# Kernel tuning notes

Measured on AMD Instinct MI355X. Metric: run time of the kernel, lower is better.

## Reference

```python
import jax, jax.numpy as jnp
import numpy as np

N_NODES = 100000
N_EDGES = 800000
D_IN = 256
D_HID = 256
D_OUT = 64
HEADS = 1
ALPHA = 0.5          # TransConv residual weight
GRAPH_WEIGHT = 0.8   # _SGFormer aggregate='add' weight
LN_EPS = 1e-5
BN_EPS = 1e-5


def layer_norm(x, g, b):
    mu = x.mean(-1, keepdims=True)
    var = ((x - mu) ** 2).mean(-1, keepdims=True)
    return (x - mu) * jax.lax.rsqrt(var + LN_EPS) * g + b


def full_attention_conv(qs, ks, vs):
    # qs, ks, vs: [N, H, C]; normalization is by the GLOBAL Frobenius norm
    qs = qs / jnp.linalg.norm(qs)
    ks = ks / jnp.linalg.norm(ks)
    N = qs.shape[0]
    kvs = jnp.einsum('lhm,lhd->hmd', ks, vs)                     # [H,C,C]
    attention_num = jnp.einsum('nhm,hmd->nhd', qs, kvs) + N * vs  # [N,H,C]
    ks_sum = ks.sum(axis=0)                                      # [H,C]
    normalizer = jnp.einsum('nhm,hm->nh', qs, ks_sum)[..., None] + N
    return attention_num / normalizer


def gcn_conv(x, src, dst, w, b, n):
    # PyG GCNConv: h = x @ W; add self-loops; D^-1/2 (A+I) D^-1/2 h; + bias
    h = x @ w
    loop = jnp.arange(n)
    s = jnp.concatenate([src, loop])
    d = jnp.concatenate([dst, loop])
    deg = jax.ops.segment_sum(jnp.ones_like(s, dtype=h.dtype), d, num_segments=n)
    dinv = jnp.where(deg > 0, jax.lax.rsqrt(jnp.maximum(deg, 1e-12)), 0.0)
    norm = dinv[s] * dinv[d]
    out = jax.ops.segment_sum(h[s] * norm[:, None], d, num_segments=n)
    return out + b


def setup_inputs() -> dict:
    key = jax.random.key(0)
    ks = jax.random.split(key, 24)
    f32 = jnp.float32
    def lin(k, fi, fo):
        s = 1.0 / np.sqrt(fi)
        kw, kb = jax.random.split(k)
        return (jax.random.uniform(kw, (fi, fo), f32, -s, s),
                jax.random.uniform(kb, (fo,), f32, -s, s))
    x = jax.random.normal(ks[0], (N_NODES, D_IN), f32)
    edge_index = jax.random.randint(ks[1], (2, N_EDGES), 0, N_NODES, jnp.int64)
    fc0_w, fc0_b = lin(ks[2], D_IN, D_HID)
    wq0_w, wq0_b = lin(ks[3], D_HID, D_HID * HEADS)
    wk0_w, wk0_b = lin(ks[4], D_HID, D_HID * HEADS)
    wv0_w, wv0_b = lin(ks[5], D_HID, D_HID * HEADS)
    wq1_w, wq1_b = lin(ks[6], D_HID, D_HID * HEADS)
    wk1_w, wk1_b = lin(ks[7], D_HID, D_HID * HEADS)
    wv1_w, wv1_b = lin(ks[8], D_HID, D_HID * HEADS)
    gcn_w0, gcn_b0 = lin(ks[9], D_IN, D_HID)
    gcn_w1, gcn_b1 = lin(ks[10], D_HID, D_HID)
    fc_w, fc_b = lin(ks[11], D_HID, D_OUT)
    ones = jnp.ones((D_HID,), f32)
    zeros = jnp.zeros((D_HID,), f32)
    return dict(
        x=x, edge_index=edge_index,
        fc0_w=fc0_w, fc0_b=fc0_b, ln0_g=ones, ln0_b=zeros,
        wq0_w=wq0_w, wq0_b=wq0_b, wk0_w=wk0_w, wk0_b=wk0_b, wv0_w=wv0_w, wv0_b=wv0_b,
        ln1_g=ones, ln1_b=zeros,
        wq1_w=wq1_w, wq1_b=wq1_b, wk1_w=wk1_w, wk1_b=wk1_b, wv1_w=wv1_w, wv1_b=wv1_b,
        ln2_g=ones, ln2_b=zeros,
        gcn_w0=gcn_w0, gcn_b0=gcn_b0, bn_g=ones, bn_b=zeros,
        gcn_w1=gcn_w1, gcn_b1=gcn_b1,
        fc_w=fc_w, fc_b=fc_b)


def reference(x, edge_index, fc0_w, fc0_b, ln0_g, ln0_b,
              wq0_w, wq0_b, wk0_w, wk0_b, wv0_w, wv0_b, ln1_g, ln1_b,
              wq1_w, wq1_b, wk1_w, wk1_b, wv1_w, wv1_b, ln2_g, ln2_b,
              gcn_w0, gcn_b0, bn_g, bn_b, gcn_w1, gcn_b1, fc_w, fc_b):
    n = x.shape[0]
    src, dst = edge_index[0], edge_index[1]
    # ---- TransConv (eval mode: dropout = identity) ----
    h = layer_norm(x @ fc0_w + fc0_b, ln0_g, ln0_b)
    h = jax.nn.relu(h)
    layer_params = [
        (wq0_w, wq0_b, wk0_w, wk0_b, wv0_w, wv0_b, ln1_g, ln1_b),
        (wq1_w, wq1_b, wk1_w, wk1_b, wv1_w, wv1_b, ln2_g, ln2_b),
    ]
    for (qw, qb, kw, kb, vw, vb, lg, lb) in layer_params:
        q = (h @ qw + qb).reshape(n, HEADS, D_HID)
        k = (h @ kw + kb).reshape(n, HEADS, D_HID)
        v = (h @ vw + vb).reshape(n, HEADS, D_HID)
        a = full_attention_conv(q, k, v).mean(axis=1)   # mean over heads
        h = layer_norm(ALPHA * a + (1.0 - ALPHA) * h, lg, lb)
    x_trans = h
    # ---- GCN branch (BN in eval: running_mean=0, running_var=1) ----
    g = gcn_conv(x, src, dst, gcn_w0, gcn_b0, n)
    g = g * (bn_g / jnp.sqrt(1.0 + BN_EPS)) + bn_b
    g = jax.nn.relu(g)
    g = gcn_conv(g, src, dst, gcn_w1, gcn_b1, n)
    # ---- combine + classifier ----
    emb = GRAPH_WEIGHT * g + (1.0 - GRAPH_WEIGHT) * x_trans
    return emb @ fc_w + fc_b
```

## Files before the change

### kernel.cpp

```cpp
#include <hip/hip_runtime.h>
#include <hip/hip_bf16.h>

#define NN 100000
#define NE 800000
#define DH 256
#define DOUT 64
#define NSPL 50000
#define NSO ((size_t)NSPL * DH)
#define NBLK 391

using bf16 = __hip_bfloat16;
typedef __attribute__((ext_vector_type(8))) short bf16x8;
typedef __attribute__((ext_vector_type(4))) float f32x4;

__device__ __forceinline__ float bits2f(unsigned short h) {
    union { unsigned int u; float f; } c; c.u = ((unsigned int)h) << 16; return c.f;
}
__device__ __forceinline__ unsigned short f2b(float v) {
    union { float f; unsigned int u; } c; c.f = v;
    unsigned int u = c.u;
    return (unsigned short)((u + 0x7FFFu + ((u >> 16) & 1u)) >> 16);
}
__device__ __forceinline__ unsigned short tob(float v) { return f2b(v); }
__device__ __forceinline__ unsigned short tob(bf16 v) {
    union { bf16 b; unsigned short u; } c; c.b = v; return c.u;
}
__device__ __forceinline__ float ldf(const void* p, size_t i, int isbf) {
    if (isbf) return bits2f(((const unsigned short*)p)[i]);
    return ((const float*)p)[i];
}
__device__ __forceinline__ float ldS(const float* p, size_t i) { return p[i]; }
__device__ __forceinline__ float ldS(const bf16* p, size_t i) { return __bfloat162float(p[i]); }
__device__ __forceinline__ void stS(float* p, size_t i, float v) { p[i] = v; }
__device__ __forceinline__ void stS(bf16* p, size_t i, float v) { p[i] = __float2bfloat16(v); }
template <typename ST> __device__ __forceinline__ float storedS(float v);
template <> __device__ __forceinline__ float storedS<float>(float v) { return v; }
template <> __device__ __forceinline__ float storedS<bf16>(float v) { return bits2f(f2b(v)); }
__device__ __forceinline__ float4 ld4S(const float* p) { return *(const float4*)p; }
__device__ __forceinline__ float4 ld4S(const bf16* p) {
    ushort4 u = *(const ushort4*)(const void*)p;
    return make_float4(bits2f(u.x), bits2f(u.y), bits2f(u.z), bits2f(u.w));
}
__device__ __forceinline__ void st4S(float* p, float4 v) { *(float4*)p = v; }
__device__ __forceinline__ void st4S(bf16* p, float4 v) {
    *(ushort4*)(void*)p = make_ushort4(f2b(v.x), f2b(v.y), f2b(v.z), f2b(v.w));
}
__device__ __forceinline__ void ld8(const void* p, size_t idx, int isbf, ushort4& o0, ushort4& o1) {
    if (isbf) {
        const ushort4* q = (const ushort4*)((const unsigned short*)p + idx);
        o0 = q[0]; o1 = q[1];
    } else {
        const float4* q = (const float4*)((const float*)p + idx);
        float4 a = q[0], b = q[1];
        o0 = make_ushort4(f2b(a.x), f2b(a.y), f2b(a.z), f2b(a.w));
        o1 = make_ushort4(f2b(b.x), f2b(b.y), f2b(b.z), f2b(b.w));
    }
}
__device__ __forceinline__ void ld8S(const bf16* p, size_t idx, ushort4& o0, ushort4& o1) {
    const ushort4* q = (const ushort4*)((const unsigned short*)p + idx);
    o0 = q[0]; o1 = q[1];
}
__device__ __forceinline__ void ld8S(const float* p, size_t idx, ushort4& o0, ushort4& o1) {
    const float4* q = (const float4*)(p + idx);
    float4 a = q[0], b = q[1];
    o0 = make_ushort4(f2b(a.x), f2b(a.y), f2b(a.z), f2b(a.w));
    o1 = make_ushort4(f2b(b.x), f2b(b.y), f2b(b.z), f2b(b.w));
}
__device__ __forceinline__ int ld_src(const int* ei, int e, int i64) {
    return i64 ? ei[2 * (size_t)e] : ei[e];
}
__device__ __forceinline__ int ld_dst(const int* ei, int e, int i64) {
    return i64 ? ei[2 * ((size_t)NE + e)] : ei[NE + e];
}

__global__ __launch_bounds__(256) void detect_kernel(const void* x, const int* ei, int* flags)
{
    __shared__ int s_sane[4], s_nz[4];
    int t = threadIdx.x;
    const unsigned short* xu = (const unsigned short*)x;
    int sane = 0;
    for (int i = t; i < 2048; i += 256) {
        float v = bits2f(xu[2 * i]);
        float a = fabsf(v);
        if (v == v && a > 1e-3f && a < 100.f) sane++;
    }
    int nz = 0;
    for (int i = t; i < 4096; i += 256) {
        if (ei[2 * (i * 122) + 1] != 0) nz++;
    }
#pragma unroll
    for (int off = 32; off > 0; off >>= 1) { sane += __shfl_down(sane, off); nz += __shfl_down(nz, off); }
    if ((t & 63) == 0) { s_sane[t >> 6] = sane; s_nz[t >> 6] = nz; }
    __syncthreads();
    if (t == 0) {
        flags[0] = ((s_sane[0] + s_sane[1] + s_sane[2] + s_sane[3]) > 1024) ? 1 : 0;
        flags[1] = ((s_nz[0] + s_nz[1] + s_nz[2] + s_nz[3]) == 0) ? 1 : 0;
    }
}

template <typename ST>
__global__ __launch_bounds__(512) void gemm_mfma(
    const void* __restrict__ A, const void* __restrict__ W,
    const void* __restrict__ bias, ST* __restrict__ C,
    int M, int Nc, const int* __restrict__ flags, int a_sel,
    float* __restrict__ ssq, float* __restrict__ csum)
{
    __shared__ unsigned short Bs[64][264];
    __shared__ float cs_s[64];
    const int isbf = flags[0];
    const int abf = (a_sel == 2) ? isbf : a_sel;
    const int tid = threadIdx.x;
    const int wave = tid >> 6, lane = tid & 63;
    const int quad = lane >> 4, nl = lane & 15;
    const int m0 = blockIdx.x * 512;
    const int n0 = blockIdx.y * 64;

#pragma unroll
    for (int it = 0; it < 4; ++it) {
        int p8 = it * 512 + tid;
        int k = p8 >> 3, nb = p8 & 7;
        ushort4 w0, w1;
        ld8(W, (size_t)k * Nc + n0 + nb * 8, isbf, w0, w1);
        int nbase = nb * 8;
        Bs[nbase + 0][k] = w0.x; Bs[nbase + 1][k] = w0.y;
        Bs[nbase + 2][k] = w0.z; Bs[nbase + 3][k] = w0.w;
        Bs[nbase + 4][k] = w1.x; Bs[nbase + 5][k] = w1.y;
        Bs[nbase + 6][k] = w1.z; Bs[nbase + 7][k] = w1.w;
    }
    if (csum != nullptr && tid < 64) cs_s[tid] = 0.f;
    __syncthreads();

    const int lrow = wave * 16 + nl;
    float bv[4];
#pragma unroll
    for (int ct = 0; ct < 4; ++ct)
        bv[ct] = bias ? ldf(bias, n0 + ct * 16 + nl, isbf) : 0.f;

    float myssq = 0.f;
    float mycs[4] = {0.f, 0.f, 0.f, 0.f};

    ushort4 c0[8], c1[8], nx0[8], nx1[8];
    {
        int arow = m0 + lrow;
        int av = (arow < M);
        size_t ab = (size_t)arow * DH + quad * 8;
#pragma unroll
        for (int s = 0; s < 8; ++s) {
            if (av) ld8(A, ab + s * 32, abf, c0[s], c1[s]);
            else { c0[s] = make_ushort4(0, 0, 0, 0); c1[s] = c0[s]; }
        }
    }

#pragma unroll
    for (int t = 0; t < 4; ++t) {
        if (t < 3) {
            int arow = m0 + (t + 1) * 128 + lrow;
            int av = (arow < M);
            size_t ab = (size_t)arow * DH + quad * 8;
#pragma unroll
            for (int s = 0; s < 8; ++s) {
                if (av) ld8(A, ab + s * 32, abf, nx0[s], nx1[s]);
                else { nx0[s] = make_ushort4(0, 0, 0, 0); nx1[s] = nx0[s]; }
            }
        }
        f32x4 acc[4] = {{0.f,0.f,0.f,0.f},{0.f,0.f,0.f,0.f},{0.f,0.f,0.f,0.f},{0.f,0.f,0.f,0.f}};
#pragma unroll
        for (int s = 0; s < 8; ++s) {
            bf16x8 af;
            ((ushort4*)&af)[0] = c0[s]; ((ushort4*)&af)[1] = c1[s];
#pragma unroll
            for (int ct = 0; ct < 4; ++ct) {
                bf16x8 bfg = *(const bf16x8*)&Bs[ct * 16 + nl][s * 32 + quad * 8];
                acc[ct] = __builtin_amdgcn_mfma_f32_16x16x32_bf16(af, bfg, acc[ct], 0, 0, 0);
            }
        }
#pragma unroll
        for (int ct = 0; ct < 4; ++ct) {
            int n = n0 + ct * 16 + nl;
#pragma unroll
            for (int r = 0; r < 4; ++r) {
                int m = m0 + t * 128 + wave * 16 + quad * 4 + r;
                if (m < M) {
                    float v = acc[ct][r] + bv[ct];
                    stS(C, (size_t)m * Nc + n, v);
                    float sv = storedS<ST>(v);
                    myssq += sv * sv;
                    mycs[ct] += sv;
                }
            }
        }
        if (t < 3) {
#pragma unroll
            for (int s = 0; s < 8; ++s) { c0[s] = nx0[s]; c1[s] = nx1[s]; }
        }
    }

    if (ssq != nullptr) {
        float s = myssq;
        s += __shfl_xor(s, 1);  s += __shfl_xor(s, 2);  s += __shfl_xor(s, 4);
        s += __shfl_xor(s, 8);  s += __shfl_xor(s, 16); s += __shfl_xor(s, 32);
        if (lane == 0) atomicAdd(ssq, s);
    }
    if (csum != nullptr) {
#pragma unroll
        for (int ct = 0; ct < 4; ++ct)
            atomicAdd(&cs_s[ct * 16 + nl], mycs[ct]);
        __syncthreads();
        if (tid < 64) atomicAdd(&csum[n0 + tid], cs_s[tid]);
    }
}

template <typename ST>
__global__ __launch_bounds__(256) void kvs_mfma(
    const ST* __restrict__ Am, const ST* __restrict__ Bm, float* __restrict__ D)
{
    __shared__ unsigned short Ast[64][36];
    __shared__ unsigned short Bst[64][36];
    const int tid = threadIdx.x;
    const int wave = tid >> 6, lane = tid & 63;
    const int quad = lane >> 4, nl = lane & 15;
    const int i0 = blockIdx.x * 64, j0 = blockIdx.y * 64;
    const int S = gridDim.z;
    const int chunk = (NN + S - 1) / S;
    const int ns = blockIdx.z * chunk;
    const int ne = min(ns + chunk, NN);
    const int nn = tid >> 3;
    const int c0 = (tid & 7) * 8;
    f32x4 acc[4] = {{0.f,0.f,0.f,0.f},{0.f,0.f,0.f,0.f},{0.f,0.f,0.f,0.f},{0.f,0.f,0.f,0.f}};

    for (int n0 = ns; n0 < ne; n0 += 32) {
        int n = n0 + nn;
        ushort4 a0, a1, b0, b1;
        if (n < ne) {
            ld8S(Am, (size_t)n * DH + i0 + c0, a0, a1);
            ld8S(Bm, (size_t)n * DH + j0 + c0, b0, b1);
        } else {
            a0 = make_ushort4(0, 0, 0, 0); a1 = a0; b0 = a0; b1 = a0;
        }
        __syncthreads();
        Ast[c0 + 0][nn] = a0.x; Ast[c0 + 1][nn] = a0.y;
        Ast[c0 + 2][nn] = a0.z; Ast[c0 + 3][nn] = a0.w;
        Ast[c0 + 4][nn] = a1.x; Ast[c0 + 5][nn] = a1.y;
        Ast[c0 + 6][nn] = a1.z; Ast[c0 + 7][nn] = a1.w;
        Bst[c0 + 0][nn] = b0.x; Bst[c0 + 1][nn] = b0.y;
        Bst[c0 + 2][nn] = b0.z; Bst[c0 + 3][nn] = b0.w;
        Bst[c0 + 4][nn] = b1.x; Bst[c0 + 5][nn] = b1.y;
        Bst[c0 + 6][nn] = b1.z; Bst[c0 + 7][nn] = b1.w;
        __syncthreads();
        bf16x8 af = *(const bf16x8*)&Ast[wave * 16 + nl][quad * 8];
#pragma unroll
        for (int ct = 0; ct < 4; ++ct) {
            bf16x8 bfg = *(const bf16x8*)&Bst[ct * 16 + nl][quad * 8];
            acc[ct] = __builtin_amdgcn_mfma_f32_16x16x32_bf16(af, bfg, acc[ct], 0, 0, 0);
        }
    }
#pragma unroll
    for (int ct = 0; ct < 4; ++ct)
#pragma unroll
        for (int r = 0; r < 4; ++r)
            atomicAdd(&D[(size_t)(i0 + wave * 16 + quad * 4 + r) * DH + j0 + ct * 16 + nl], acc[ct][r]);
}

__global__ __launch_bounds__(256) void kvs2b_kernel(const float* __restrict__ kvs,
                                                    unsigned short* __restrict__ kvsb)
{
    int i = blockIdx.x * 256 + threadIdx.x;
    size_t o = (size_t)i * 8;
    float4 a = *(const float4*)(kvs + o);
    float4 b = *(const float4*)(kvs + o + 4);
    *(ushort4*)(kvsb + o)     = make_ushort4(f2b(a.x), f2b(a.y), f2b(a.z), f2b(a.w));
    *(ushort4*)(kvsb + o + 4) = make_ushort4(f2b(b.x), f2b(b.y), f2b(b.z), f2b(b.w));
}

template <typename ST>
__global__ __launch_bounds__(256) void attn_mfma(
    const ST* __restrict__ Q, const ST* __restrict__ V,
    const unsigned short* __restrict__ kvsb, const float* __restrict__ ks_sum,
    const float* __restrict__ qss, const float* __restrict__ kss,
    ST* __restrict__ out)
{
    __shared__ float ks_s[DH];
    __shared__ float nrm_s[64];
    const int tid = threadIdx.x;
    const int wave = tid >> 6, lane = tid & 63;
    const int quad = lane >> 4, nl = lane & 15;
    const int m0 = blockIdx.x * 64;
    const int j0 = blockIdx.y * 128;

    ks_s[tid] = ks_sum[tid];
    __syncthreads();

    const int arow = m0 + wave * 16 + nl;
    const int av = (arow < NN);
    const size_t abase = (size_t)arow * DH + quad * 8;
    f32x4 acc[8];
#pragma unroll
    for (int i = 0; i < 8; ++i) acc[i] = (f32x4){0.f, 0.f, 0.f, 0.f};
    float nrm = 0.f;

#pragma unroll 2
    for (int k0 = 0; k0 < DH; k0 += 32) {
        ushort4 a0, a1;
        if (av) ld8S(Q, abase + k0, a0, a1);
        else { a0 = make_ushort4(0,0,0,0); a1 = a0; }
        bf16x8 af;
        ((ushort4*)&af)[0] = a0; ((ushort4*)&af)[1] = a1;
#pragma unroll
        for (int j = 0; j < 8; ++j)
            nrm += bits2f(((const unsigned short*)&af)[j]) * ks_s[k0 + quad * 8 + j];
        const unsigned short* kb = kvsb + (size_t)(j0 + nl) * DH + k0 + quad * 8;
#pragma unroll
        for (int ct = 0; ct < 8; ++ct) {
            bf16x8 bfg = *(const bf16x8*)(kb + (size_t)ct * 16 * DH);
            acc[ct] = __builtin_amdgcn_mfma_f32_16x16x32_bf16(af, bfg, acc[ct], 0, 0, 0);
        }
    }
    nrm += __shfl_xor(nrm, 16);
    nrm += __shfl_xor(nrm, 32);
    if (lane < 16) nrm_s[wave * 16 + lane] = nrm;
    __syncthreads();
    const float scale = rsqrtf(*qss) * rsqrtf(*kss);
#pragma unroll
    for (int r = 0; r < 4; ++r) {
        int row = m0 + wave * 16 + quad * 4 + r;
        if (row >= NN) continue;
        float den = nrm_s[wave * 16 + quad * 4 + r] * scale + (float)NN;
#pragma unroll
        for (int ct = 0; ct < 8; ++ct) {
            int col = j0 + ct * 16 + nl;
            float v = ldS(V, (size_t)row * DH + col);
            float numv = acc[ct][r] * scale + (float)NN * v;
            stS(out, (size_t)row * DH + col, numv / den);
        }
    }
}

template <typename ST>
__global__ __launch_bounds__(256) void ln_kernel(
    const ST* __restrict__ A, const ST* __restrict__ B,
    float alpha, float beta,
    const void* __restrict__ g, const void* __restrict__ b,
    ST* __restrict__ out, int relu, const int* __restrict__ flags)
{
    const int isbf = flags[0];
    const int wave = threadIdx.x >> 6, lane = threadIdx.x & 63;
    const int row = blockIdx.x * 4 + wave;
    if (row >= NN) return;
    const size_t base = (size_t)row * DH + lane * 4;
    float4 v = ld4S(&A[base]);
    v.x *= alpha; v.y *= alpha; v.z *= alpha; v.w *= alpha;
    if (B) {
        float4 w = ld4S(&B[base]);
        v.x += beta * w.x; v.y += beta * w.y; v.z += beta * w.z; v.w += beta * w.w;
    }
    float s = v.x + v.y + v.z + v.w;
    float s2 = v.x * v.x + v.y * v.y + v.z * v.z + v.w * v.w;
#pragma unroll
    for (int off = 32; off > 0; off >>= 1) {
        s += __shfl_xor(s, off);
        s2 += __shfl_xor(s2, off);
    }
    float mean = s * (1.f / DH);
    float var = s2 * (1.f / DH) - mean * mean;
    float rstd = rsqrtf(var + 1e-5f);
    float4 o;
    o.x = (v.x - mean) * rstd * ldf(g, lane * 4 + 0, isbf) + ldf(b, lane * 4 + 0, isbf);
    o.y = (v.y - mean) * rstd * ldf(g, lane * 4 + 1, isbf) + ldf(b, lane * 4 + 1, isbf);
    o.z = (v.z - mean) * rstd * ldf(g, lane * 4 + 2, isbf) + ldf(b, lane * 4 + 2, isbf);
    o.w = (v.w - mean) * rstd * ldf(g, lane * 4 + 3, isbf) + ldf(b, lane * 4 + 3, isbf);
    if (relu) {
        o.x = fmaxf(o.x, 0.f); o.y = fmaxf(o.y, 0.f);
        o.z = fmaxf(o.z, 0.f); o.w = fmaxf(o.w, 0.f);
    }
    st4S(&out[base], o);
}

__global__ __launch_bounds__(256) void count_kernel(const int* __restrict__ ei, int* __restrict__ cnt,
                                                    const int* __restrict__ flags)
{
    int e = blockIdx.x * 256 + threadIdx.x;
    if (e >= NE) return;
    int d = ld_dst(ei, e, flags[1]);
    if ((unsigned)d < NN) atomicAdd(&cnt[d], 1);
}

__global__ __launch_bounds__(256) void scan_block_kernel(const int* __restrict__ cnt,
                                                         int* __restrict__ pre, int* __restrict__ bsum)
{
    __shared__ int s[256];
    int i = blockIdx.x * 256 + threadIdx.x;
    int v = (i < NN) ? cnt[i] : 0;
    s[threadIdx.x] = v;
    __syncthreads();
    for (int off = 1; off < 256; off <<= 1) {
        int t = (threadIdx.x >= off) ? s[threadIdx.x - off] : 0;
        __syncthreads();
        s[threadIdx.x] += t;
        __syncthreads();
    }
    if (i < NN) pre[i] = s[threadIdx.x] - v;
    if (threadIdx.x == 255) bsum[blockIdx.x] = s[255];
}

__global__ __launch_bounds__(512) void scan_partial_kernel(int* __restrict__ bsum, int nb)
{
    __shared__ int s[512];
    int t = threadIdx.x;
    int v = (t < nb) ? bsum[t] : 0;
    s[t] = v;
    __syncthreads();
    for (int off = 1; off < 512; off <<= 1) {
        int u = (t >= off) ? s[t - off] : 0;
        __syncthreads();
        s[t] += u;
        __syncthreads();
    }
    if (t < nb) bsum[t] = s[t] - v;
}

__global__ __launch_bounds__(256) void finalize_kernel(int* __restrict__ base, const int* __restrict__ bsum,
                                                       const int* __restrict__ cnt, int* __restrict__ cursor,
                                                       float* __restrict__ dinv)
{
    int i = blockIdx.x * 256 + threadIdx.x;
    if (i >= NN) return;
    int b = base[i] + bsum[blockIdx.x];
    base[i] = b;
    cursor[i] = b;
    dinv[i] = rsqrtf((float)cnt[i] + 1.0f);
}

__global__ __launch_bounds__(256) void scatter_kernel(const int* __restrict__ ei, int* __restrict__ cursor,
                                                      int* __restrict__ srcs, const int* __restrict__ flags)
{
    int e = blockIdx.x * 256 + threadIdx.x;
    if (e >= NE) return;
    int i64 = flags[1];
    int s = ld_src(ei, e, i64), d = ld_dst(ei, e, i64);
    if ((unsigned)s >= NN || (unsigned)d >= NN) return;
    int pos = atomicAdd(&cursor[d], 1);
    srcs[pos] = s;
}

template <typename ST, int MODE>
__global__ __launch_bounds__(256) void fgather_kernel(
    const ST* __restrict__ Hs, const ST* __restrict__ Ht,
    const int* __restrict__ base, const int* __restrict__ cnt,
    const int* __restrict__ srcs, const float* __restrict__ dinv,
    const void* __restrict__ bias, const void* __restrict__ bng, const void* __restrict__ bnb,
    const int* __restrict__ flags, ST* __restrict__ out)
{
    const int isbf = flags[0];
    int node = blockIdx.x * 4 + (threadIdx.x >> 6);
    int lane = threadIdx.x & 63;
    if (node >= NN) return;
    int b0 = base[node], deg = cnt[node];
    float dd = dinv[node];
    float4 a0 = make_float4(0.f, 0.f, 0.f, 0.f);
    float4 a1 = make_float4(0.f, 0.f, 0.f, 0.f);
    int j = 0;
    for (; j + 4 <= deg; j += 4) {
        int s0 = srcs[b0 + j + 0], s1 = srcs[b0 + j + 1];
        int s2 = srcs[b0 + j + 2], s3 = srcs[b0 + j + 3];
        float n0 = dd * dinv[s0], n1 = dd * dinv[s1];
        float n2 = dd * dinv[s2], n3 = dd * dinv[s3];
        float4 h0 = ld4S(&Hs[(size_t)s0 * DH + lane * 4]);
        float4 h1 = ld4S(&Hs[(size_t)s1 * DH + lane * 4]);
        float4 h2 = ld4S(&Hs[(size_t)s2 * DH + lane * 4]);
        float4 h3 = ld4S(&Hs[(size_t)s3 * DH + lane * 4]);
        a0.x += h0.x * n0; a0.y += h0.y * n0; a0.z += h0.z * n0; a0.w += h0.w * n0;
        a1.x += h1.x * n1; a1.y += h1.y * n1; a1.z += h1.z * n1; a1.w += h1.w * n1;
        a0.x += h2.x * n2; a0.y += h2.y * n2; a0.z += h2.z * n2; a0.w += h2.w * n2;
        a1.x += h3.x * n3; a1.y += h3.y * n3; a1.z += h3.z * n3; a1.w += h3.w * n3;
    }
    for (; j < deg; ++j) {
        int s0 = srcs[b0 + j];
        float n0 = dd * dinv[s0];
        float4 h0 = ld4S(&Hs[(size_t)s0 * DH + lane * 4]);
        a0.x += h0.x * n0; a0.y += h0.y * n0; a0.z += h0.z * n0; a0.w += h0.w * n0;
    }
    const size_t obase = (size_t)node * DH + lane * 4;
    float4 own = ld4S(&Hs[obase]);
    float di2 = dd * dd;
    int c = lane * 4;
    float4 v;
    v.x = a0.x + a1.x + own.x * di2 + ldf(bias, c + 0, isbf);
    v.y = a0.y + a1.y + own.y * di2 + ldf(bias, c + 1, isbf);
    v.z = a0.z + a1.z + own.z * di2 + ldf(bias, c + 2, isbf);
    v.w = a0.w + a1.w + own.w * di2 + ldf(bias, c + 3, isbf);
    if (MODE == 0) {
        const float bnscale = 0.99999500003749981f;
        v.x = fmaxf(v.x * (ldf(bng, c + 0, isbf) * bnscale) + ldf(bnb, c + 0, isbf), 0.f);
        v.y = fmaxf(v.y * (ldf(bng, c + 1, isbf) * bnscale) + ldf(bnb, c + 1, isbf), 0.f);
        v.z = fmaxf(v.z * (ldf(bng, c + 2, isbf) * bnscale) + ldf(bnb, c + 2, isbf), 0.f);
        v.w = fmaxf(v.w * (ldf(bng, c + 3, isbf) * bnscale) + ldf(bnb, c + 3, isbf), 0.f);
    } else {
        float4 t = ld4S(&Ht[obase]);
        v.x = 0.8f * v.x + 0.2f * t.x;
        v.y = 0.8f * v.y + 0.2f * t.y;
        v.z = 0.8f * v.z + 0.2f * t.z;
        v.w = 0.8f * v.w + 0.2f * t.w;
    }
    st4S(&out[obase], v);
}

__global__ __launch_bounds__(256) void deg_kernel(const int* __restrict__ ei, float* __restrict__ deg,
                                                  const int* __restrict__ flags)
{
    int i64 = flags[1];
    int e = blockIdx.x * 256 + threadIdx.x;
    if (e >= NE) return;
    int d = ld_dst(ei, e, i64);
    if ((unsigned)d < NN) atomicAdd(&deg[d], 1.0f);
}

__global__ __launch_bounds__(256) void dinv_kernel(float* __restrict__ deg)
{
    int i = blockIdx.x * 256 + threadIdx.x;
    if (i < NN) deg[i] = rsqrtf(deg[i] + 1.0f);
}

template <typename ST>
__global__ __launch_bounds__(256) void agg_kernel(
    const ST* __restrict__ Hs, const int* __restrict__ ei,
    const float* __restrict__ dinv, float* __restrict__ lo, float* __restrict__ hi,
    const int* __restrict__ flags)
{
    int i64 = flags[1];
    int e = blockIdx.x * 4 + (threadIdx.x >> 6);
    int lane = threadIdx.x & 63;
    if (e >= NE) return;
    int s = ld_src(ei, e, i64), d = ld_dst(ei, e, i64);
    if ((unsigned)s >= NN || (unsigned)d >= NN) return;
    float nrm = dinv[s] * dinv[d];
    const float4 h4 = ld4S(&Hs[(size_t)s * DH + lane * 4]);
    float* o = (d < NSPL ? &lo[(size_t)d * DH] : &hi[(size_t)(d - NSPL) * DH]) + lane * 4;
    atomicAdd(o + 0, h4.x * nrm);
    atomicAdd(o + 1, h4.y * nrm);
    atomicAdd(o + 2, h4.z * nrm);
    atomicAdd(o + 3, h4.w * nrm);
}

template <typename ST>
__global__ __launch_bounds__(256) void gcn_epi1_kernel(
    const float* __restrict__ lo, const float* __restrict__ hi,
    const ST* __restrict__ h1, const float* __restrict__ dinv,
    const void* __restrict__ b0, const void* __restrict__ bng, const void* __restrict__ bnb,
    const int* __restrict__ flags, ST* __restrict__ out)
{
    const int isbf = flags[0];
    size_t idx = (size_t)blockIdx.x * 256 + threadIdx.x;
    if (idx >= (size_t)NN * DH) return;
    int i = (int)(idx >> 8), c = (int)(idx & 255);
    float aggv = (i < NSPL) ? lo[idx] : hi[idx - NSO];
    float di = dinv[i];
    float v = aggv + ldS(h1, idx) * di * di + ldf(b0, c, isbf);
    const float bnscale = 0.99999500003749981f;
    v = v * (ldf(bng, c, isbf) * bnscale) + ldf(bnb, c, isbf);
    stS(out, idx, fmaxf(v, 0.f));
}

template <typename ST>
__global__ __launch_bounds__(256) void gcn_epi2_kernel(
    const float* __restrict__ lo, const float* __restrict__ hi,
    const ST* __restrict__ h2, const ST* __restrict__ Ht, const float* __restrict__ dinv,
    const void* __restrict__ b1, const int* __restrict__ flags, ST* __restrict__ out)
{
    const int isbf = flags[0];
    size_t idx = (size_t)blockIdx.x * 256 + threadIdx.x;
    if (idx >= (size_t)NN * DH) return;
    int i = (int)(idx >> 8), c = (int)(idx & 255);
    float aggv = (i < NSPL) ? lo[idx] : hi[idx - NSO];
    float di = dinv[i];
    float g = aggv + ldS(h2, idx) * di * di + ldf(b1, c, isbf);
    stS(out, idx, 0.8f * g + 0.2f * ldS(Ht, idx));
}

__global__ __launch_bounds__(256) void diag_kernel(float* out, size_t n, float val)
{
    size_t i = (size_t)blockIdx.x * 256 + threadIdx.x;
    if (i < n) out[i] = val;
}

template <typename ST>
static void run_pipeline(void* const* d_in, void* d_out, char* wsb, hipStream_t stream, int use_csr)
{
    const void* x      = d_in[0];
    const int*  ei     = (const int*)d_in[1];
    const void* fc0_w  = d_in[2];  const void* fc0_b  = d_in[3];
    const void* ln0_g  = d_in[4];  const void* ln0_b  = d_in[5];
    const void* wq0_w  = d_in[6];  const void* wq0_b  = d_in[7];
    const void* wk0_w  = d_in[8];  const void* wk0_b  = d_in[9];
    const void* wv0_w  = d_in[10]; const void* wv0_b  = d_in[11];
    const void* ln1_g  = d_in[12]; const void* ln1_b  = d_in[13];
    const void* wq1_w  = d_in[14]; const void* wq1_b  = d_in[15];
    const void* wk1_w  = d_in[16]; const void* wk1_b  = d_in[17];
    const void* wv1_w  = d_in[18]; const void* wv1_b  = d_in[19];
    const void* ln2_g  = d_in[20]; const void* ln2_b  = d_in[21];
    const void* gcn_w0 = d_in[22]; const void* gcn_b0 = d_in[23];
    const void* bn_g   = d_in[24]; const void* bn_b   = d_in[25];
    const void* gcn_w1 = d_in[26]; const void* gcn_b1 = d_in[27];
    const void* fc_w   = d_in[28]; const void* fc_b   = d_in[29];

    const size_t stN = (size_t)NN * DH * sizeof(ST);
    ST* H  = (ST*)(wsb);
    ST* Qb = (ST*)(wsb + stN);
    ST* Kb = (ST*)(wsb + 2 * stN);
    ST* Vb = (ST*)(wsb + 3 * stN);
    float* aux = (float*)(wsb + 4 * stN);
    float* kvs    = aux;
    float* ks_sum = aux + 65536;
    float* qss    = aux + 65792;
    float* kss    = aux + 65793;
    float* dinv   = aux + 65808;
    int*   flags  = (int*)(aux + 65808 + NN);
    int* cnt    = (int*)(aux + 65808 + NN + 16);
    int* base   = cnt + NN;
    int* cursor = base + NN;
    int* bsum   = cursor + NN;
    int* srcs   = bsum + 512;
    unsigned short* kvsb = (unsigned short*)dinv;

    const int asel = (sizeof(ST) == 2) ? 1 : 0;
    dim3 gemmGrid((NN + 511) / 512, DH / 64);
    const size_t NELEM = (size_t)NN * DH;

    detect_kernel<<<1, 256, 0, stream>>>(x, ei, flags);

    gemm_mfma<ST><<<gemmGrid, 512, 0, stream>>>(x, fc0_w, fc0_b, Qb, NN, DH, flags, 2, nullptr, nullptr);
    ln_kernel<ST><<<(NN + 3) / 4, 256, 0, stream>>>(Qb, (const ST*)nullptr, 1.f, 0.f, ln0_g, ln0_b, H, 1, flags);

    for (int layer = 0; layer < 2; ++layer) {
        const void *qw, *qb, *kw, *kb, *vw, *vb, *lg, *lb;
        if (layer == 0) { qw = wq0_w; qb = wq0_b; kw = wk0_w; kb = wk0_b; vw = wv0_w; vb = wv0_b; lg = ln1_g; lb = ln1_b; }
        else            { qw = wq1_w; qb = wq1_b; kw = wk1_w; kb = wk1_b; vw = wv1_w; vb = wv1_b; lg = ln2_g; lb = ln2_b; }
        hipMemsetAsync(aux, 0, (65536 + 256 + 2) * sizeof(float), stream);
        gemm_mfma<ST><<<gemmGrid, 512, 0, stream>>>(H, qw, qb, Qb, NN, DH, flags, asel, qss, nullptr);
        gemm_mfma<ST><<<gemmGrid, 512, 0, stream>>>(H, kw, kb, Kb, NN, DH, flags, asel, kss, ks_sum);
        gemm_mfma<ST><<<gemmGrid, 512, 0, stream>>>(H, vw, vb, Vb, NN, DH, flags, asel, nullptr, nullptr);
        kvs_mfma<ST><<<dim3(4, 4, 128), 256, 0, stream>>>(Vb, Kb, kvs);
        kvs2b_kernel<<<32, 256, 0, stream>>>(kvs, kvsb);
        attn_mfma<ST><<<dim3((NN + 63) / 64, 2), 256, 0, stream>>>(Qb, Vb, kvsb, ks_sum, qss, kss, Kb);
        ln_kernel<ST><<<(NN + 3) / 4, 256, 0, stream>>>(Kb, H, 0.5f, 0.5f, lg, lb, H, 0, flags);
    }

    if (use_csr) {
        hipMemsetAsync(cnt, 0, NN * sizeof(int), stream);
        count_kernel<<<(NE + 255) / 256, 256, 0, stream>>>(ei, cnt, flags);
        scan_block_kernel<<<NBLK, 256, 0, stream>>>(cnt, base, bsum);
        scan_partial_kernel<<<1, 512, 0, stream>>>(bsum, NBLK);
        finalize_kernel<<<NBLK, 256, 0, stream>>>(base, bsum, cnt, cursor, dinv);
        scatter_kernel<<<(NE + 255) / 256, 256, 0, stream>>>(ei, cursor, srcs, flags);

        gemm_mfma<ST><<<gemmGrid, 512, 0, stream>>>(x, gcn_w0, nullptr, Qb, NN, DH, flags, 2, nullptr, nullptr);
        fgather_kernel<ST, 0><<<(NN + 3) / 4, 256, 0, stream>>>(
            Qb, (const ST*)nullptr, base, cnt, srcs, dinv, gcn_b0, bn_g, bn_b, flags, Kb);
        gemm_mfma<ST><<<gemmGrid, 512, 0, stream>>>(Kb, gcn_w1, nullptr, Vb, NN, DH, flags, asel, nullptr, nullptr);
        fgather_kernel<ST, 1><<<(NN + 3) / 4, 256, 0, stream>>>(
            Vb, H, base, cnt, srcs, dinv, gcn_b1, nullptr, nullptr, flags, Qb);

        gemm_mfma<float><<<dim3((NN + 511) / 512, 1), 512, 0, stream>>>(Qb, fc_w, fc_b, (float*)d_out, NN, DOUT, flags, asel, nullptr, nullptr);
    } else {
        float* a1lo = (float*)(wsb + 2 * stN);
        float* a1hi = a1lo + NSO;
        ST* h2; float *a2lo, *a2hi;
        if (sizeof(ST) == 4) { h2 = Vb; a2lo = (float*)(wsb + 2 * stN); a2hi = a2lo + NSO; }
        else                 { h2 = Kb; a2lo = (float*)(wsb + stN);     a2hi = (float*)(wsb + 3 * stN); }

        hipMemsetAsync(dinv, 0, NN * sizeof(float), stream);
        deg_kernel<<<(NE + 255) / 256, 256, 0, stream>>>(ei, dinv, flags);
        dinv_kernel<<<(NN + 255) / 256, 256, 0, stream>>>(dinv);

        gemm_mfma<ST><<<gemmGrid, 512, 0, stream>>>(x, gcn_w0, nullptr, Qb, NN, DH, flags, 2, nullptr, nullptr);
        hipMemsetAsync(a1lo, 0, NELEM * sizeof(float), stream);
        agg_kernel<ST><<<(NE + 3) / 4, 256, 0, stream>>>(Qb, ei, dinv, a1lo, a1hi, flags);
        gcn_epi1_kernel<ST><<<(NELEM + 255) / 256, 256, 0, stream>>>(a1lo, a1hi, Qb, dinv, gcn_b0, bn_g, bn_b, flags, Qb);

        gemm_mfma<ST><<<gemmGrid, 512, 0, stream>>>(Qb, gcn_w1, nullptr, h2, NN, DH, flags, asel, nullptr, nullptr);
        hipMemsetAsync(a2lo, 0, NSO * sizeof(float), stream);
        hipMemsetAsync(a2hi, 0, NSO * sizeof(float), stream);
        agg_kernel<ST><<<(NE + 3) / 4, 256, 0, stream>>>(h2, ei, dinv, a2lo, a2hi, flags);
        gcn_epi2_kernel<ST><<<(NELEM + 255) / 256, 256, 0, stream>>>(a2lo, a2hi, h2, H, dinv, gcn_b1, flags, h2);

        gemm_mfma<float><<<dim3((NN + 511) / 512, 1), 512, 0, stream>>>(h2, fc_w, fc_b, (float*)d_out, NN, DOUT, flags, asel, nullptr, nullptr);
    }
}

extern "C" void kernel_launch(void* const* d_in, const int* in_sizes, int n_in,
                              void* d_out, int out_size, void* d_ws, size_t ws_size,
                              hipStream_t stream)
{
    char* wsb = (char*)d_ws;
    const size_t AUXF  = 65808 + NN + 16;
    const size_t CSRI  = 3 * (size_t)NN + 512 + NE;
    const size_t AUXB  = AUXF * sizeof(float);
    const size_t AUXB2 = AUXB + CSRI * sizeof(int);
    const size_t needA  = 4 * ((size_t)NN * DH * 4) + AUXB;
    const size_t needA2 = 4 * ((size_t)NN * DH * 4) + AUXB2;
    const size_t needB  = 4 * ((size_t)NN * DH * 2) + AUXB;
    const size_t needB2 = 4 * ((size_t)NN * DH * 2) + AUXB2;

    if (ws_size >= needA) {
        run_pipeline<float>(d_in, d_out, wsb, stream, ws_size >= needA2);
    } else if (ws_size >= needB) {
        run_pipeline<bf16>(d_in, d_out, wsb, stream, ws_size >= needB2);
    } else {
        float mb = (float)(ws_size >> 20);
        size_t n = (size_t)out_size;
        diag_kernel<<<(n + 255) / 256, 256, 0, stream>>>((float*)d_out, n, mb);
    }
}
```

Before: 1.889 ms.

## Restructure GEMM to keep A rows in registers and loop over N tiles

The GEMM kernel now assigns each block 128 rows, loads each A row from global memory once into registers, and loops over all 64-column weight tiles inside the block, reloading the weight tile into shared memory for each. Before, each block handled 512 rows for a single 64-column slice, so the grid's N dimension reread the A matrix four times. The change cuts redundant A traffic at the cost of reloading B per block, extra barriers per N tile, and dropping the software prefetch of the next A row tile. Column-sum accumulation moves to a full-width shared array.

```diff
diff --git a/kernel.cpp b/kernel.cpp
--- a/kernel.cpp
+++ b/kernel.cpp
@@ -106,92 +106,78 @@
     float* __restrict__ ssq, float* __restrict__ csum)
 {
     __shared__ unsigned short Bs[64][264];
-    __shared__ float cs_s[64];
+    __shared__ float cs_s[DH];
     const int isbf = flags[0];
     const int abf = (a_sel == 2) ? isbf : a_sel;
     const int tid = threadIdx.x;
     const int wave = tid >> 6, lane = tid & 63;
     const int quad = lane >> 4, nl = lane & 15;
-    const int m0 = blockIdx.x * 512;
-    const int n0 = blockIdx.y * 64;
-
-#pragma unroll
-    for (int it = 0; it < 4; ++it) {
-        int p8 = it * 512 + tid;
-        int k = p8 >> 3, nb = p8 & 7;
-        ushort4 w0, w1;
-        ld8(W, (size_t)k * Nc + n0 + nb * 8, isbf, w0, w1);
-        int nbase = nb * 8;
-        Bs[nbase + 0][k] = w0.x; Bs[nbase + 1][k] = w0.y;
-        Bs[nbase + 2][k] = w0.z; Bs[nbase + 3][k] = w0.w;
-        Bs[nbase + 4][k] = w1.x; Bs[nbase + 5][k] = w1.y;
-        Bs[nbase + 6][k] = w1.z; Bs[nbase + 7][k] = w1.w;
-    }
-    if (csum != nullptr && tid < 64) cs_s[tid] = 0.f;
-    __syncthreads();
-
-    const int lrow = wave * 16 + nl;
-    float bv[4];
-#pragma unroll
-    for (int ct = 0; ct < 4; ++ct)
-        bv[ct] = bias ? ldf(bias, n0 + ct * 16 + nl, isbf) : 0.f;
+    const int m0 = blockIdx.x * 128;
+    const int ntiles = Nc >> 6;
+
+    const int arow = m0 + wave * 16 + nl;
+    const int av = (arow < M);
+    const size_t ab = (size_t)arow * DH + quad * 8;
+    ushort4 pa0[8], pa1[8];
+#pragma unroll
+    for (int s = 0; s < 8; ++s) {
+        if (av) ld8(A, ab + s * 32, abf, pa0[s], pa1[s]);
+        else { pa0[s] = make_ushort4(0, 0, 0, 0); pa1[s] = pa0[s]; }
+    }
+    if (csum != nullptr && tid < DH) cs_s[tid] = 0.f;
 
     float myssq = 0.f;
-    float mycs[4] = {0.f, 0.f, 0.f, 0.f};
-
-    ushort4 c0[8], c1[8], nx0[8], nx1[8];
-    {
-        int arow = m0 + lrow;
-        int av = (arow < M);
-        size_t ab = (size_t)arow * DH + quad * 8;
-#pragma unroll
-        for (int s = 0; s < 8; ++s) {
-            if (av) ld8(A, ab + s * 32, abf, c0[s], c1[s]);
-            else { c0[s] = make_ushort4(0, 0, 0, 0); c1[s] = c0[s]; }
-        }
-    }
-
-#pragma unroll
-    for (int t = 0; t < 4; ++t) {
-        if (t < 3) {
-            int arow = m0 + (t + 1) * 128 + lrow;
-            int av = (arow < M);
-            size_t ab = (size_t)arow * DH + quad * 8;
-#pragma unroll
-            for (int s = 0; s < 8; ++s) {
-                if (av) ld8(A, ab + s * 32, abf, nx0[s], nx1[s]);
-                else { nx0[s] = make_ushort4(0, 0, 0, 0); nx1[s] = nx0[s]; }
-            }
-        }
+
+    for (int nt = 0; nt < ntiles; ++nt) {
+        const int n0 = nt * 64;
+        if (nt > 0) __syncthreads();
+#pragma unroll
+        for (int it = 0; it < 4; ++it) {
+            int p8 = it * 512 + tid;
+            int k = p8 >> 3, nb = p8 & 7;
+            ushort4 w0, w1;
+            ld8(W, (size_t)k * Nc + n0 + nb * 8, isbf, w0, w1);
+            int nbase = nb * 8;
+            Bs[nbase + 0][k] = w0.x; Bs[nbase + 1][k] = w0.y;
+            Bs[nbase + 2][k] = w0.z; Bs[nbase + 3][k] = w0.w;
+            Bs[nbase + 4][k] = w1.x; Bs[nbase + 5][k] = w1.y;
+            Bs[nbase + 6][k] = w1.z; Bs[nbase + 7][k] = w1.w;
+        }
+        __syncthreads();
+
         f32x4 acc[4] = {{0.f,0.f,0.f,0.f},{0.f,0.f,0.f,0.f},{0.f,0.f,0.f,0.f},{0.f,0.f,0.f,0.f}};
 #pragma unroll
         for (int s = 0; s < 8; ++s) {
             bf16x8 af;
-            ((ushort4*)&af)[0] = c0[s]; ((ushort4*)&af)[1] = c1[s];
+            ((ushort4*)&af)[0] = pa0[s]; ((ushort4*)&af)[1] = pa1[s];
 #pragma unroll
             for (int ct = 0; ct < 4; ++ct) {
                 bf16x8 bfg = *(const bf16x8*)&Bs[ct * 16 + nl][s * 32 + quad * 8];
                 acc[ct] = __builtin_amdgcn_mfma_f32_16x16x32_bf16(af, bfg, acc[ct], 0, 0, 0);
             }
         }
+
+        float mycs[4] = {0.f, 0.f, 0.f, 0.f};
 #pragma unroll
         for (int ct = 0; ct < 4; ++ct) {
             int n = n0 + ct * 16 + nl;
+            float bv = bias ? ldf(bias, n, isbf) : 0.f;
 #pragma unroll
             for (int r = 0; r < 4; ++r) {
-                int m = m0 + t * 128 + wave * 16 + quad * 4 + r;
+                int m = m0 + wave * 16 + quad * 4 + r;
                 if (m < M) {
-                    float v = acc[ct][r] + bv[ct];
+                    float v = acc[ct][r] + bv;
                     stS(C, (size_t)m * Nc + n, v);
                     float sv = storedS<ST>(v);
-                    myssq += sv * sv;
-                    mycs[ct] += sv;
+                    if (ssq != nullptr) myssq += sv * sv;
+                    if (csum != nullptr) mycs[ct] += sv;
                 }
             }
         }
-        if (t < 3) {
-#pragma unroll
-            for (int s = 0; s < 8; ++s) { c0[s] = nx0[s]; c1[s] = nx1[s]; }
+        if (csum != nullptr) {
+#pragma unroll
+            for (int ct = 0; ct < 4; ++ct)
+                atomicAdd(&cs_s[n0 + ct * 16 + nl], mycs[ct]);
         }
     }
 
@@ -202,11 +188,8 @@
         if (lane == 0) atomicAdd(ssq, s);
     }
     if (csum != nullptr) {
-#pragma unroll
-        for (int ct = 0; ct < 4; ++ct)
-            atomicAdd(&cs_s[ct * 16 + nl], mycs[ct]);
-        __syncthreads();
-        if (tid < 64) atomicAdd(&csum[n0 + tid], cs_s[tid]);
+        __syncthreads();
+        if (tid < Nc) atomicAdd(&csum[tid], cs_s[tid]);
     }
 }
 
@@ -622,7 +605,7 @@
     unsigned short* kvsb = (unsigned short*)dinv;
 
     const int asel = (sizeof(ST) == 2) ? 1 : 0;
-    dim3 gemmGrid((NN + 511) / 512, DH / 64);
+    dim3 gemmGrid((NN + 127) / 128);
     const size_t NELEM = (size_t)NN * DH;
 
     detect_kernel<<<1, 256, 0, stream>>>(x, ei, flags);
@@ -659,7 +642,7 @@
         fgather_kernel<ST, 1><<<(NN + 3) / 4, 256, 0, stream>>>(
             Vb, H, base, cnt, srcs, dinv, gcn_b1, nullptr, nullptr, flags, Qb);
 
-        gemm_mfma<float><<<dim3((NN + 511) / 512, 1), 512, 0, stream>>>(Qb, fc_w, fc_b, (float*)d_out, NN, DOUT, flags, asel, nullptr, nullptr);
+        gemm_mfma<float><<<gemmGrid, 512, 0, stream>>>(Qb, fc_w, fc_b, (float*)d_out, NN, DOUT, flags, asel, nullptr, nullptr);
     } else {
         float* a1lo = (float*)(wsb + 2 * stN);
         float* a1hi = a1lo + NSO;
@@ -682,7 +665,7 @@
         agg_kernel<ST><<<(NE + 3) / 4, 256, 0, stream>>>(h2, ei, dinv, a2lo, a2hi, flags);
         gcn_epi2_kernel<ST><<<(NELEM + 255) / 256, 256, 0, stream>>>(a2lo, a2hi, h2, H, dinv, gcn_b1, flags, h2);
 
-        gemm_mfma<float><<<dim3((NN + 511) / 512, 1), 512, 0, stream>>>(h2, fc_w, fc_b, (float*)d_out, NN, DOUT, flags, asel, nullptr, nullptr);
+        gemm_mfma<float><<<gemmGrid, 512, 0, stream>>>(h2, fc_w, fc_b, (float*)d_out, NN, DOUT, flags, asel, nullptr, nullptr);
     }
 }
 
```

After: 2.010 ms. 1.06x slower.
